# Kernel tuning notes

Measured on AMD Instinct MI355X. Metric: run time of the kernel, lower is better.

The kernel has to match this reference:

```python
import jax, jax.numpy as jnp
import numpy as np

N, E = 4096, 8192
IN_V, OUT_V, IN_E = 512, 512, 128
A_COEF = 0.5  # self.a; self.b = 1 - a


def setup_inputs() -> dict:
    key = jax.random.key(0)
    ks = jax.random.split(key, 8)
    stdv = 1.0 / np.sqrt(OUT_V)
    return {
        "H_v": jax.random.normal(ks[0], (N, IN_V), jnp.float32),
        "H_e": jax.random.normal(ks[1], (E, IN_E), jnp.float32),
        "adj_e": jax.random.uniform(ks[2], (E, E), jnp.float32),
        "adj_v": jax.random.uniform(ks[3], (N, N), jnp.float32),
        "T": jax.random.uniform(ks[4], (N, E), jnp.float32),
        "weight": jax.random.uniform(ks[5], (IN_V, OUT_V), jnp.float32, -stdv, stdv),
        "p": jax.random.normal(ks[6], (1, IN_E), jnp.float32),
        "bias": jax.random.uniform(ks[7], (OUT_V,), jnp.float32, -stdv, stdv),
    }


def reference(H_v, H_e, adj_e, adj_v, T, weight, p, bias):
    # node_layer=True path.
    # edge scaling vector: (H_e @ p^T) -> [E]
    e_scale = (H_e @ p.T)[:, 0]
    # T @ diag(e_scale) @ T^T, fusing the diagonal as column scaling of T
    multiplier1 = (T * e_scale[None, :]) @ T.T  # [N, N]
    # M1 = eye*1 + (1-eye)*multiplier1  == set diagonal to 1
    idx = jnp.arange(multiplier1.shape[0])
    M1 = multiplier1.at[idx, idx].set(1.0)
    adjusted_A = M1 * adj_v
    output = (adjusted_A @ H_v) @ weight
    output1 = (adj_v @ H_v) @ weight
    out = output * A_COEF + output1 * (1.0 - A_COEF)
    ret = out + bias
    return (ret, H_e)
```

## Files before the change

### kernel.cpp

```cpp
#include <hip/hip_runtime.h>
#include <hip/hip_bf16.h>
#include <stdint.h>

#define N_NODES 4096
#define N_EDGES 8192
#define IN_V    512
#define OUT_V   512
#define IN_E    128

typedef __bf16 bf16;
typedef __bf16 bf16x8 __attribute__((ext_vector_type(8)));
typedef __bf16 bf16x4 __attribute__((ext_vector_type(4)));
typedef float  f32x4  __attribute__((ext_vector_type(4)));

__device__ __forceinline__ void g2l16(const void* g, void* l) {
    __builtin_amdgcn_global_load_lds(
        (const __attribute__((address_space(1))) void*)g,
        (__attribute__((address_space(3))) void*)l,
        16, 0, 0);
}

__global__ void escale_k(const float* __restrict__ He, const float* __restrict__ p,
                         float* __restrict__ es) {
    const int row  = blockIdx.x * 4 + (threadIdx.x >> 6);
    const int lane = threadIdx.x & 63;
    const float* r = He + (size_t)row * IN_E;
    float v = r[lane] * p[lane] + r[lane + 64] * p[lane + 64];
#pragma unroll
    for (int off = 32; off > 0; off >>= 1) v += __shfl_down(v, off);
    if (lane == 0) es[row] = v;
}

__global__ void conv_T(const float* __restrict__ T, const float* __restrict__ es,
                       bf16* __restrict__ Ts, bf16* __restrict__ Tb) {
    const size_t i4 = (size_t)blockIdx.x * 256 + threadIdx.x;
    const f32x4 t = ((const f32x4*)T)[i4];
    const int  c4 = (int)(i4 & (N_EDGES / 4 - 1));
    const f32x4 s = ((const f32x4*)es)[c4];
    bf16x4 tb, ts;
#pragma unroll
    for (int j = 0; j < 4; j++) { tb[j] = (bf16)t[j]; ts[j] = (bf16)(t[j] * s[j]); }
    ((bf16x4*)Tb)[i4] = tb;
    ((bf16x4*)Ts)[i4] = ts;
}

__global__ void conv_bf16(const float* __restrict__ in, bf16* __restrict__ o) {
    const size_t i4 = (size_t)blockIdx.x * 256 + threadIdx.x;
    const f32x4 t = ((const f32x4*)in)[i4];
    bf16x4 v;
#pragma unroll
    for (int j = 0; j < 4; j++) v[j] = (bf16)t[j];
    ((bf16x4*)o)[i4] = v;
}

__global__ void transW(const float* __restrict__ W, bf16* __restrict__ Wt) {
    const int idx = blockIdx.x * 256 + threadIdx.x;
    const int j = idx >> 9, k = idx & 511;
    Wt[idx] = (bf16)W[k * OUT_V + j];
}

__global__ void bias_init(const float* __restrict__ bias, float* __restrict__ o) {
    const int idx = blockIdx.x * 256 + threadIdx.x;
    o[idx] = bias[idx & (OUT_V - 1)];
}

template <int EPI>
__global__ __launch_bounds__(256, 3) void gemm_bt(
    const bf16* __restrict__ A, const bf16* __restrict__ B,
    const float* __restrict__ aux, void* __restrict__ out,
    int M, int N, int K, int KS) {
    __shared__ __align__(16) bf16 As[128 * 32];
    __shared__ __align__(16) bf16 Bs[128 * 32];
    const int tid  = threadIdx.x;
    const int wave = tid >> 6;
    const int lane = tid & 63;

    int bx, by;
    if constexpr (EPI == 1) {
        int idx = blockIdx.x;
        bx = (int)((sqrtf(8.0f * (float)idx + 1.0f) - 1.0f) * 0.5f);
        while ((bx + 1) * (bx + 2) / 2 <= idx) bx++;
        while (bx * (bx + 1) / 2 > idx) bx--;
        by = idx - bx * (bx + 1) / 2;
    } else {
        bx = blockIdx.x;
        by = blockIdx.y;
    }
    const int bm0 = bx * 128;
    const int bn0 = by * 128;
    const int wr  = (wave >> 1) * 64;
    const int wc  = (wave & 1) * 64;

    const int sr = wave * 16 + (lane >> 2);
    const int sb = (lane & 3) * 16;
    const char* Ab0 = (const char*)A + (size_t)(bm0 + sr) * K * 2 + sb;
    const char* Ab1 = (const char*)A + (size_t)(bm0 + sr + 64) * K * 2 + sb;
    const char* Bb0 = (const char*)B + (size_t)(bn0 + sr) * K * 2 + sb;
    const char* Bb1 = (const char*)B + (size_t)(bn0 + sr + 64) * K * 2 + sb;
    char* AsW0 = (char*)As + wave * 1024;
    char* AsW1 = AsW0 + 4096;
    char* BsW0 = (char*)Bs + wave * 1024;
    char* BsW1 = BsW0 + 4096;

    f32x4 acc[4][4];
#pragma unroll
    for (int i = 0; i < 4; i++)
#pragma unroll
        for (int j = 0; j < 4; j++) acc[i][j] = f32x4{0.f, 0.f, 0.f, 0.f};

    const int a_off = (wr + (lane & 15)) * 32 + (lane >> 4) * 8;
    const int b_off = (wc + (lane & 15)) * 32 + (lane >> 4) * 8;

    const int k_beg = blockIdx.z * KS;
    const int k_end = k_beg + KS;
    for (int k0 = k_beg; k0 < k_end; k0 += 32) {
        const size_t kb = (size_t)k0 * 2;
        g2l16(Ab0 + kb, AsW0);
        g2l16(Ab1 + kb, AsW1);
        g2l16(Bb0 + kb, BsW0);
        g2l16(Bb1 + kb, BsW1);
        __syncthreads();

        bf16x8 a[4], b[4];
#pragma unroll
        for (int mt = 0; mt < 4; mt++) a[mt] = *(const bf16x8*)(As + a_off + mt * (16 * 32));
#pragma unroll
        for (int nt = 0; nt < 4; nt++) b[nt] = *(const bf16x8*)(Bs + b_off + nt * (16 * 32));
#pragma unroll
        for (int mt = 0; mt < 4; mt++)
#pragma unroll
            for (int nt = 0; nt < 4; nt++)
                acc[mt][nt] = __builtin_amdgcn_mfma_f32_16x16x32_bf16(
                    a[mt], b[nt], acc[mt][nt], 0, 0, 0);
        __syncthreads();
    }

    const int col = lane & 15;
    const int r0  = (lane >> 4) * 4;
#pragma unroll
    for (int mt = 0; mt < 4; mt++) {
#pragma unroll
        for (int nt = 0; nt < 4; nt++) {
            const int gn = bn0 + wc + nt * 16 + col;
#pragma unroll
            for (int r = 0; r < 4; r++) {
                const int gm = bm0 + wr + mt * 16 + r0 + r;
                const float c = acc[mt][nt][r];
                if constexpr (EPI == 0) {
                    ((bf16*)out)[(size_t)gm * N + gn] = (bf16)c;
                } else if constexpr (EPI == 1) {
                    const float av = aux[(size_t)gm * N + gn];
                    const float v  = (gm == gn) ? 2.0f * av : (c + 1.0f) * av;
                    ((bf16*)out)[(size_t)gm * N + gn] = (bf16)v;
                } else {
                    atomicAdd(&((float*)out)[(size_t)gm * N + gn], 0.5f * c);
                }
            }
            if constexpr (EPI == 1) {
                if (bm0 != bn0) {
                    const int gm0 = bm0 + wr + mt * 16 + r0;
                    const size_t tb = (size_t)gn * N + gm0;
                    const f32x4 at = *(const f32x4*)(aux + tb);
                    bf16x4 v;
#pragma unroll
                    for (int r = 0; r < 4; r++) v[r] = (bf16)((acc[mt][nt][r] + 1.0f) * at[r]);
                    *(bf16x4*)((bf16*)out + tb) = v;
                }
            }
        }
    }
}

extern "C" void kernel_launch(void* const* d_in, const int* in_sizes, int n_in,
                              void* d_out, int out_size, void* d_ws, size_t ws_size,
                              hipStream_t stream) {
    const float* H_v   = (const float*)d_in[0];
    const float* H_e   = (const float*)d_in[1];
    const float* adj_v = (const float*)d_in[3];
    const float* T     = (const float*)d_in[4];
    const float* W     = (const float*)d_in[5];
    const float* p     = (const float*)d_in[6];
    const float* bias  = (const float*)d_in[7];
    float* out = (float*)d_out;

    char* ws = (char*)d_ws;
    float* es  = (float*)(ws);
    bf16*  Ts  = (bf16*)(ws + 32768);
    bf16*  Tb  = (bf16*)(ws + 32768 + 67108864ull);
    bf16*  A2  = (bf16*)(ws + 32768 + 134217728ull);
    bf16*  Hvb = (bf16*)(ws + 32768 + 167772160ull);
    bf16*  Wt  = (bf16*)(ws + 32768 + 171966464ull);
    bf16*  HwT = (bf16*)(ws + 32768 + 172490752ull);

    escale_k<<<N_EDGES / 4, 256, 0, stream>>>(H_e, p, es);
    conv_T<<<(int)(((size_t)N_NODES * N_EDGES / 4) / 256), 256, 0, stream>>>(T, es, Ts, Tb);
    conv_bf16<<<(N_NODES * IN_V / 4) / 256, 256, 0, stream>>>(H_v, Hvb);
    transW<<<(IN_V * OUT_V) / 256, 256, 0, stream>>>(W, Wt);
    hipMemcpyAsync(out + (size_t)N_NODES * OUT_V, H_e,
                   (size_t)N_EDGES * IN_E * sizeof(float),
                   hipMemcpyDeviceToDevice, stream);
    bias_init<<<(N_NODES * OUT_V) / 256, 256, 0, stream>>>(bias, out);
    gemm_bt<0><<<dim3(IN_V / 128, N_NODES / 128), 256, 0, stream>>>(
        Wt, Hvb, nullptr, HwT, IN_V, N_NODES, IN_V, IN_V);
    gemm_bt<1><<<dim3((32 * 33) / 2, 1, 1), 256, 0, stream>>>(
        Ts, Tb, adj_v, A2, N_NODES, N_NODES, N_EDGES, N_EDGES);
    gemm_bt<2><<<dim3(N_NODES / 128, OUT_V / 128, 4), 256, 0, stream>>>(
        A2, HwT, nullptr, out, N_NODES, OUT_V, N_NODES, N_NODES / 4);
}
```

Baseline: 798.0 us.

## Double-buffer LDS in GEMM, swizzle triangular block order, replace atomics with partial-sum reduce

```diff
diff --git a/kernel.cpp b/kernel.cpp
--- a/kernel.cpp
+++ b/kernel.cpp
@@ -59,9 +59,19 @@
     Wt[idx] = (bf16)W[k * OUT_V + j];
 }
 
-__global__ void bias_init(const float* __restrict__ bias, float* __restrict__ o) {
-    const int idx = blockIdx.x * 256 + threadIdx.x;
-    o[idx] = bias[idx & (OUT_V - 1)];
+__global__ void finalize_k(const float* __restrict__ part, const float* __restrict__ bias,
+                           float* __restrict__ out) {
+    const size_t i4  = (size_t)blockIdx.x * 256 + threadIdx.x;
+    const size_t npp = (size_t)N_NODES * OUT_V / 4;
+    const f32x4 b  = ((const f32x4*)bias)[i4 & (OUT_V / 4 - 1)];
+    const f32x4 s0 = ((const f32x4*)part)[i4];
+    const f32x4 s1 = ((const f32x4*)part)[i4 + npp];
+    const f32x4 s2 = ((const f32x4*)part)[i4 + 2 * npp];
+    const f32x4 s3 = ((const f32x4*)part)[i4 + 3 * npp];
+    f32x4 r;
+#pragma unroll
+    for (int j = 0; j < 4; j++) r[j] = b[j] + 0.5f * ((s0[j] + s1[j]) + (s2[j] + s3[j]));
+    ((f32x4*)out)[i4] = r;
 }
 
 template <int EPI>
@@ -69,15 +79,16 @@
     const bf16* __restrict__ A, const bf16* __restrict__ B,
     const float* __restrict__ aux, void* __restrict__ out,
     int M, int N, int K, int KS) {
-    __shared__ __align__(16) bf16 As[128 * 32];
-    __shared__ __align__(16) bf16 Bs[128 * 32];
+    __shared__ __align__(16) bf16 As[2][128 * 32];
+    __shared__ __align__(16) bf16 Bs[2][128 * 32];
     const int tid  = threadIdx.x;
     const int wave = tid >> 6;
     const int lane = tid & 63;
 
     int bx, by;
     if constexpr (EPI == 1) {
-        int idx = blockIdx.x;
+        int idx = (int)blockIdx.x;
+        idx = (idx & 7) * 66 + (idx >> 3);
         bx = (int)((sqrtf(8.0f * (float)idx + 1.0f) - 1.0f) * 0.5f);
         while ((bx + 1) * (bx + 2) / 2 <= idx) bx++;
         while (bx * (bx + 1) / 2 > idx) bx--;
@@ -97,10 +108,7 @@
     const char* Ab1 = (const char*)A + (size_t)(bm0 + sr + 64) * K * 2 + sb;
     const char* Bb0 = (const char*)B + (size_t)(bn0 + sr) * K * 2 + sb;
     const char* Bb1 = (const char*)B + (size_t)(bn0 + sr + 64) * K * 2 + sb;
-    char* AsW0 = (char*)As + wave * 1024;
-    char* AsW1 = AsW0 + 4096;
-    char* BsW0 = (char*)Bs + wave * 1024;
-    char* BsW1 = BsW0 + 4096;
+    const int woff = wave * 1024;
 
     f32x4 acc[4][4];
 #pragma unroll
@@ -111,32 +119,44 @@
     const int a_off = (wr + (lane & 15)) * 32 + (lane >> 4) * 8;
     const int b_off = (wc + (lane & 15)) * 32 + (lane >> 4) * 8;
 
-    const int k_beg = blockIdx.z * KS;
-    const int k_end = k_beg + KS;
-    for (int k0 = k_beg; k0 < k_end; k0 += 32) {
-        const size_t kb = (size_t)k0 * 2;
-        g2l16(Ab0 + kb, AsW0);
-        g2l16(Ab1 + kb, AsW1);
-        g2l16(Bb0 + kb, BsW0);
-        g2l16(Bb1 + kb, BsW1);
-        __syncthreads();
-
+    auto do_stage = [&](bf16* AsB, bf16* BsB, size_t kb) {
+        g2l16(Ab0 + kb, (char*)AsB + woff);
+        g2l16(Ab1 + kb, (char*)AsB + woff + 4096);
+        g2l16(Bb0 + kb, (char*)BsB + woff);
+        g2l16(Bb1 + kb, (char*)BsB + woff + 4096);
+    };
+    auto do_mfma = [&](const bf16* AsB, const bf16* BsB) {
         bf16x8 a[4], b[4];
 #pragma unroll
-        for (int mt = 0; mt < 4; mt++) a[mt] = *(const bf16x8*)(As + a_off + mt * (16 * 32));
-#pragma unroll
-        for (int nt = 0; nt < 4; nt++) b[nt] = *(const bf16x8*)(Bs + b_off + nt * (16 * 32));
+        for (int mt = 0; mt < 4; mt++) a[mt] = *(const bf16x8*)(AsB + a_off + mt * 512);
+#pragma unroll
+        for (int nt = 0; nt < 4; nt++) b[nt] = *(const bf16x8*)(BsB + b_off + nt * 512);
 #pragma unroll
         for (int mt = 0; mt < 4; mt++)
 #pragma unroll
             for (int nt = 0; nt < 4; nt++)
                 acc[mt][nt] = __builtin_amdgcn_mfma_f32_16x16x32_bf16(
                     a[mt], b[nt], acc[mt][nt], 0, 0, 0);
+    };
+
+    const int k_beg = (int)blockIdx.z * KS;
+    const int k_end = k_beg + KS;
+    do_stage(As[0], Bs[0], (size_t)k_beg * 2);
+    __syncthreads();
+    for (int k0 = k_beg; k0 < k_end; k0 += 64) {
+        if (k0 + 32 < k_end) do_stage(As[1], Bs[1], (size_t)(k0 + 32) * 2);
+        do_mfma(As[0], Bs[0]);
+        __syncthreads();
+        if (k0 + 64 < k_end) do_stage(As[0], Bs[0], (size_t)(k0 + 64) * 2);
+        do_mfma(As[1], Bs[1]);
         __syncthreads();
     }
 
     const int col = lane & 15;
     const int r0  = (lane >> 4) * 4;
+    float* po = nullptr;
+    if constexpr (EPI == 3)
+        po = (float*)out + (size_t)blockIdx.z * ((size_t)M * (size_t)N);
 #pragma unroll
     for (int mt = 0; mt < 4; mt++) {
 #pragma unroll
@@ -153,7 +173,7 @@
                     const float v  = (gm == gn) ? 2.0f * av : (c + 1.0f) * av;
                     ((bf16*)out)[(size_t)gm * N + gn] = (bf16)v;
                 } else {
-                    atomicAdd(&((float*)out)[(size_t)gm * N + gn], 0.5f * c);
+                    po[(size_t)gm * N + gn] = c;
                 }
             }
             if constexpr (EPI == 1) {
@@ -191,6 +211,7 @@
     bf16*  Hvb = (bf16*)(ws + 32768 + 167772160ull);
     bf16*  Wt  = (bf16*)(ws + 32768 + 171966464ull);
     bf16*  HwT = (bf16*)(ws + 32768 + 172490752ull);
+    float* part = (float*)(ws + 32768);
 
     escale_k<<<N_EDGES / 4, 256, 0, stream>>>(H_e, p, es);
     conv_T<<<(int)(((size_t)N_NODES * N_EDGES / 4) / 256), 256, 0, stream>>>(T, es, Ts, Tb);
@@ -199,11 +220,11 @@
     hipMemcpyAsync(out + (size_t)N_NODES * OUT_V, H_e,
                    (size_t)N_EDGES * IN_E * sizeof(float),
                    hipMemcpyDeviceToDevice, stream);
-    bias_init<<<(N_NODES * OUT_V) / 256, 256, 0, stream>>>(bias, out);
     gemm_bt<0><<<dim3(IN_V / 128, N_NODES / 128), 256, 0, stream>>>(
         Wt, Hvb, nullptr, HwT, IN_V, N_NODES, IN_V, IN_V);
     gemm_bt<1><<<dim3((32 * 33) / 2, 1, 1), 256, 0, stream>>>(
         Ts, Tb, adj_v, A2, N_NODES, N_NODES, N_EDGES, N_EDGES);
-    gemm_bt<2><<<dim3(N_NODES / 128, OUT_V / 128, 4), 256, 0, stream>>>(
-        A2, HwT, nullptr, out, N_NODES, OUT_V, N_NODES, N_NODES / 4);
-}
+    gemm_bt<3><<<dim3(N_NODES / 128, OUT_V / 128, 4), 256, 0, stream>>>(
+        A2, HwT, nullptr, part, N_NODES, OUT_V, N_NODES, N_NODES / 4);
+    finalize_k<<<(N_NODES * OUT_V / 4) / 256, 256, 0, stream>>>(part, bias, out);
+}
```

After: 715.7 us. 10.3% less time.
